# Performance work log

Measured on AMD Instinct MI355X. Metric: run time of the kernel, lower is better.

## Reference

```python
import jax, jax.numpy as jnp
import numpy as np
from jax import lax

IOU_THRESHOLD = 0.5
TOP = 1000


def setup_inputs() -> dict:
    key = jax.random.key(0)
    k1, k2, k3, k4, k5 = jax.random.split(key, 5)
    B, P = 16, 20000
    # valid (x1, y1, x2, y2) boxes on an ~800x800 image
    x1 = jax.random.uniform(k1, (B, P)) * 800.0
    y1 = jax.random.uniform(k2, (B, P)) * 800.0
    w = jax.random.uniform(k3, (B, P)) * 200.0 + 1.0
    h = jax.random.uniform(k4, (B, P)) * 200.0 + 1.0
    reg = jnp.stack([x1, y1, x1 + w, y1 + h], axis=-1)  # [B, P, 4]
    cls = jax.random.normal(k5, (B, P))                  # [B, P]
    return {"reg": reg, "cls": cls}


def _pairwise_iou(boxes):
    """boxes: [B, N, 4] (x1,y1,x2,y2) -> IoU [B, N, N]."""
    a = boxes[:, :, None, :]  # [B, N, 1, 4]
    b = boxes[:, None, :, :]  # [B, 1, N, 4]
    xx1 = jnp.maximum(a[..., 0], b[..., 0])
    yy1 = jnp.maximum(a[..., 1], b[..., 1])
    xx2 = jnp.minimum(a[..., 2], b[..., 2])
    yy2 = jnp.minimum(a[..., 3], b[..., 3])
    inter = jnp.clip(xx2 - xx1, 0.0) * jnp.clip(yy2 - yy1, 0.0)
    area_a = (a[..., 2] - a[..., 0]) * (a[..., 3] - a[..., 1])
    area_b = (b[..., 2] - b[..., 0]) * (b[..., 3] - b[..., 1])
    return inter / (area_a + area_b - inter)


def reference(reg, cls):
    B = cls.shape[0]
    # sort by confidence descending, gather boxes, keep top
    order = jnp.argsort(-cls, axis=1)                      # [B, P]
    sorted_cls = jnp.take_along_axis(cls, order, axis=1)[:, :TOP]            # [B, N]
    sorted_reg = jnp.take_along_axis(reg, order[:, :, None], axis=1)[:, :TOP]  # [B, N, 4]
    N = sorted_cls.shape[1]

    iou = _pairwise_iou(sorted_reg)                        # [B, N, N]

    # sequential greedy suppression: if box i still kept, drop boxes with IoU>=thr
    def body(mask, i):
        keep_i = mask[:, i]                                # [B]
        tmp = iou[:, i, :] < IOU_THRESHOLD                 # [B, N]
        upd = (mask & tmp).at[:, i].set(True)
        new_mask = jnp.where(keep_i[:, None], upd, mask)
        return new_mask, None

    mask0 = jnp.ones((B, N), dtype=bool)
    mask, _ = lax.scan(body, mask0, jnp.arange(N))

    out_reg = jnp.where(mask[:, :, None], sorted_reg, 0.0)
    out_cls = jnp.where(mask, sorted_cls, 0.0)
    return out_reg, out_cls
```

## Files before the change

kernel.cpp:

```cpp
#include <hip/hip_runtime.h>
#include <stdint.h>

#define BATCH 16
#define NPTS  20000
#define TOPK  1000
#define NKPT  20
#define NBIN  2048
#define NCOPY 4
#define CANDCAP 1024

__device__ __forceinline__ uint32_t key_desc(float f) {
    uint32_t u = __float_as_uint(f);
    uint32_t m = (u & 0x80000000u) ? ~u : (u | 0x80000000u);
    return ~m;
}

__device__ __forceinline__ float key_undo(uint32_t k) {
    uint32_t m = ~k;
    uint32_t u = (m & 0x80000000u) ? (m & 0x7FFFFFFFu) : ~m;
    return __uint_as_float(u);
}

__device__ __forceinline__ void push64(bool pred, uint64_t val, int* cntr,
                                       uint64_t* list, int lane) {
    uint64_t mask = __ballot(pred);
    if (mask) {
        int first = __ffsll((long long)mask) - 1;
        int base = 0;
        if (lane == first) base = atomicAdd(cntr, (int)__popcll(mask));
        base = __shfl(base, first);
        if (pred) {
            int off = (int)__popcll(mask & ((1ull << lane) - 1ull));
            list[base + off] = val;
        }
    }
}

__device__ __forceinline__ void wave_select(const uint64_t* lst, int n, int r,
                                            uint64_t* out, int wave, int lane) {
    if (wave == 0) {
        uint64_t my = (lane < n) ? lst[lane] : ~0ull;
        int rank = 0;
        for (int i = 0; i < n; ++i) { uint64_t o = __shfl(my, i); if (o < my) rank++; }
        if (lane < n && rank == r) *out = my;
    }
}

__device__ uint64_t bit_search(const uint32_t* klds, uint64_t known, uint64_t kmask,
                               int startbit, uint32_t r, int* sh_c,
                               int tid, int lane) {
    for (int bit = startbit; bit >= 0; --bit) {
        if (tid == 0) *sh_c = 0;
        __syncthreads();
        uint32_t local = 0;
        #pragma unroll
        for (int j = 0; j < NKPT; ++j) {
            int p = tid + j * 1024;
            if (p < NPTS) {
                uint64_t k64 = ((uint64_t)klds[p] << 32) | (uint32_t)p;
                if ((k64 & kmask) == known && !((k64 >> bit) & 1ull)) local++;
            }
        }
        #pragma unroll
        for (int d = 1; d < 64; d <<= 1) local += __shfl_xor(local, d);
        if (lane == 0 && local) atomicAdd(sh_c, (int)local);
        __syncthreads();
        uint32_t c0 = (uint32_t)*sh_c;
        if (r >= c0) { known |= 1ull << bit; r -= c0; }
        kmask |= 1ull << bit;
        __syncthreads();
    }
    return known;
}

__device__ __forceinline__ void hist_scan_find(
    uint32_t (*wh)[NBIN], uint32_t* wsum, uint32_t* wpre,
    int* sh_T, int* sh_r, int* sh_binc,
    int tid, int wave, int lane, uint32_t r)
{
    uint32_t m0 = 0, m1 = 0;
    #pragma unroll
    for (int cpy = 0; cpy < NCOPY; ++cpy) { m0 += wh[cpy][2*tid]; m1 += wh[cpy][2*tid+1]; }
    uint32_t s = m0 + m1, x = s;
    #pragma unroll
    for (int d = 1; d < 64; d <<= 1) { uint32_t t = __shfl_up(x, d); if (lane >= d) x += t; }
    if (lane == 63) wsum[wave] = x;
    __syncthreads();
    if (wave == 0 && lane < 16) {
        uint32_t v = wsum[lane], y = v;
        #pragma unroll
        for (int d = 1; d < 16; d <<= 1) { uint32_t t = __shfl_up(y, d); if (lane >= d) y += t; }
        wpre[lane] = y - v;
    }
    __syncthreads();
    uint32_t e = wpre[wave] + (x - s);
    if (r >= e && r < e + s) {
        if (r < e + m0) { *sh_T = 2*tid;     *sh_r = (int)(r - e);      *sh_binc = (int)m0; }
        else            { *sh_T = 2*tid + 1; *sh_r = (int)(r - e - m0); *sh_binc = (int)m1; }
    }
}

__global__ __launch_bounds__(1024) void topk_kernel(
    const float* __restrict__ reg, const float* __restrict__ cls,
    float4* __restrict__ ws_boxes, float* __restrict__ ws_cls)
{
    __shared__ uint32_t klds[NPTS];
    __shared__ uint32_t whist[NCOPY][NBIN];
    __shared__ uint32_t mpre[NBIN];
    __shared__ uint32_t bcnt[NBIN];
    __shared__ uint64_t bucket[1024];
    __shared__ uint64_t cand[CANDCAP];
    __shared__ uint64_t cand2[64];
    __shared__ uint32_t wsum[16], wpre16[16];
    __shared__ int      sh_T, sh_r, sh_binc, sh_cnt, sh_c;
    __shared__ uint64_t sh_kthkey;

    const int b = blockIdx.x, tid = threadIdx.x;
    const int wave = tid >> 6, lane = tid & 63;
    const float* c = cls + (size_t)b * NPTS;

    #pragma unroll
    for (int i = 0; i < NCOPY * NBIN / 1024; ++i) ((uint32_t*)whist)[tid + i * 1024] = 0;
    __syncthreads();
    #pragma unroll
    for (int j = 0; j < NKPT; ++j) {
        int p = tid + j * 1024;
        if (p < NPTS) {
            uint32_t k = key_desc(c[p]);
            klds[p] = k;
            atomicAdd(&whist[wave >> 2][k >> 21], 1u);
        }
    }
    __syncthreads();

    {
        uint32_t m0 = 0, m1 = 0;
        #pragma unroll
        for (int cpy = 0; cpy < NCOPY; ++cpy) { m0 += whist[cpy][2*tid]; m1 += whist[cpy][2*tid+1]; }
        uint32_t s = m0 + m1, x = s;
        #pragma unroll
        for (int d = 1; d < 64; d <<= 1) { uint32_t t = __shfl_up(x, d); if (lane >= d) x += t; }
        if (lane == 63) wsum[wave] = x;
        __syncthreads();
        if (wave == 0 && lane < 16) {
            uint32_t v = wsum[lane], y = v;
            #pragma unroll
            for (int d = 1; d < 16; d <<= 1) { uint32_t t = __shfl_up(y, d); if (lane >= d) y += t; }
            wpre16[lane] = y - v;
        }
        __syncthreads();
        uint32_t E = wpre16[wave] + (x - s);
        mpre[2*tid]   = E;
        mpre[2*tid+1] = E + m0;
        bcnt[2*tid] = 0; bcnt[2*tid+1] = 0;
        uint32_t r9 = TOPK - 1;
        if (r9 >= E && r9 < E + s) {
            if (r9 < E + m0) { sh_T = 2*tid;     sh_r = (int)(r9 - E);      sh_binc = (int)m0; }
            else             { sh_T = 2*tid + 1; sh_r = (int)(r9 - E - m0); sh_binc = (int)m1; }
        }
    }
    __syncthreads();
    const uint32_t T1 = (uint32_t)sh_T;
    int r = sh_r;
    const int cnt1 = sh_binc;
    uint64_t known = (uint64_t)T1 << 53;

    if (cnt1 <= 64) {
        if (tid == 0) sh_cnt = 0;
        __syncthreads();
        #pragma unroll
        for (int j = 0; j < NKPT; ++j) {
            int p = tid + j * 1024;
            uint32_t k = (p < NPTS) ? klds[p] : 0xFFFFFFFFu;
            push64(p < NPTS && (k >> 21) == T1,
                   ((uint64_t)k << 32) | (uint32_t)p, &sh_cnt, cand2, lane);
        }
        __syncthreads();
        wave_select(cand2, cnt1, r, &sh_kthkey, wave, lane);
        __syncthreads();
    } else if (cnt1 <= CANDCAP) {
        if (tid == 0) sh_cnt = 0;
        __syncthreads();
        #pragma unroll
        for (int j = 0; j < NKPT; ++j) {
            int p = tid + j * 1024;
            uint32_t k = (p < NPTS) ? klds[p] : 0xFFFFFFFFu;
            push64(p < NPTS && (k >> 21) == T1,
                   ((uint64_t)k << 32) | (uint32_t)p, &sh_cnt, cand, lane);
        }
        __syncthreads();
        #pragma unroll
        for (int i = 0; i < NCOPY * NBIN / 1024; ++i) ((uint32_t*)whist)[tid + i * 1024] = 0;
        __syncthreads();
        for (int i = tid; i < cnt1; i += 1024)
            atomicAdd(&whist[wave >> 2][(uint32_t)((cand[i] >> 42) & 2047)], 1u);
        __syncthreads();
        hist_scan_find(whist, wsum, wpre16, &sh_T, &sh_r, &sh_binc, tid, wave, lane, (uint32_t)r);
        __syncthreads();
        const uint32_t T2 = (uint32_t)sh_T; r = sh_r;
        const int cnt2 = sh_binc;
        known |= (uint64_t)T2 << 42;
        if (cnt2 <= 64) {
            if (tid == 0) sh_cnt = 0;
            __syncthreads();
            for (int i = tid; i < cnt1; i += 1024)
                push64(((cand[i] >> 42) & 2047) == (uint64_t)T2,
                       cand[i], &sh_cnt, cand2, lane);
            __syncthreads();
            wave_select(cand2, cnt2, r, &sh_kthkey, wave, lane);
            __syncthreads();
        } else {
            uint64_t kk = bit_search(klds, known, 0xFFFFFC0000000000ull, 41,
                                     (uint32_t)r, &sh_c, tid, lane);
            if (tid == 0) sh_kthkey = kk;
            __syncthreads();
        }
    } else {
        uint64_t kk = bit_search(klds, known, 0xFFE0000000000000ull, 52,
                                 (uint32_t)r, &sh_c, tid, lane);
        if (tid == 0) sh_kthkey = kk;
        __syncthreads();
    }
    const uint64_t kthkey = sh_kthkey;

    #pragma unroll
    for (int j = 0; j < NKPT; ++j) {
        int p = tid + j * 1024;
        if (p < NPTS) {
            uint32_t k = klds[p];
            uint64_t key = ((uint64_t)k << 32) | (uint32_t)p;
            if (key <= kthkey) {
                uint32_t t = k >> 21;
                uint32_t pos = mpre[t] + atomicAdd(&bcnt[t], 1u);
                bucket[pos] = key;
            }
        }
    }
    __syncthreads();

    if (tid < TOPK) {
        uint64_t e = bucket[tid];
        uint32_t t = (uint32_t)(e >> 53);
        uint32_t base = mpre[t], n = bcnt[t];
        int rank = (int)base;
        for (uint32_t q = 0; q < n; ++q) rank += (bucket[base + q] < e) ? 1 : 0;
        int p = (int)(e & 0xFFFFFFFFull);
        ws_boxes[b * TOPK + rank] = ((const float4*)reg)[(size_t)b * NPTS + p];
        ws_cls[b * TOPK + rank] = key_undo((uint32_t)(e >> 32));
    }
}

__global__ __launch_bounds__(256) void iou_kernel(
    const float4* __restrict__ ws_boxes, uint32_t* __restrict__ suppT)
{
    __shared__ float4 boxes[TOPK];
    __shared__ float  areas[TOPK];
    const int b   = blockIdx.y;
    const int j   = blockIdx.x;
    const int tid = threadIdx.x;
    for (int i = tid; i < TOPK; i += 256) {
        float4 v = ws_boxes[b * TOPK + i];
        boxes[i] = v;
        areas[i] = (v.z - v.x) * (v.w - v.y);
    }
    __syncthreads();

    const int lane = tid & 63;
    const int wave = tid >> 6;
    uint32_t* t = suppT + (size_t)b * 32 * 1024;

    for (int k = wave; ; k += 4) {
        const int i = j + (k << 4);
        if (i >= TOPK) break;
        float4 a = boxes[i];
        float areaA = areas[i];
        uint64_t mine = 0;
        for (int w2 = i >> 6; w2 < 16; ++w2) {
            int col = (w2 << 6) | lane;
            bool sup = false;
            if (col < TOPK) {
                float4 bb = boxes[col];
                float xx1 = fmaxf(a.x, bb.x);
                float yy1 = fmaxf(a.y, bb.y);
                float xx2 = fminf(a.z, bb.z);
                float yy2 = fminf(a.w, bb.w);
                float iw = fmaxf(xx2 - xx1, 0.0f);
                float ih = fmaxf(yy2 - yy1, 0.0f);
                float inter = iw * ih;
                float iou = inter / (areaA + areas[col] - inter);
                sup = (iou >= 0.5f);
            }
            uint64_t m = __ballot(sup);
            if (lane == w2) mine = m;
        }
        if (lane < 16) {
            t[(2 * lane + 0) * 1024 + i] = (uint32_t)(mine & 0xFFFFFFFFull);
            t[(2 * lane + 1) * 1024 + i] = (uint32_t)(mine >> 32);
        }
    }
}

__global__ __launch_bounds__(64) void sweep_kernel(
    const uint32_t* __restrict__ suppT, const float4* __restrict__ ws_boxes,
    const float* __restrict__ ws_cls, float* __restrict__ out)
{
    const int b    = blockIdx.x;
    const int lane = threadIdx.x;
    const int myw  = lane & 31;
    const uint32_t* base = suppT + (size_t)b * 32 * 1024;

    uint32_t remv = 0, keptw = 0;
    uint4 dgA[8], clA[8], dgB[8], clB[8];

#define LOADG(W, DG, CL) { \
    const uint4* dp_ = (const uint4*)(base + (W) * 1024 + (W) * 32); \
    const uint4* cp_ = (const uint4*)(base + myw * 1024 + (W) * 32); \
    _Pragma("unroll") \
    for (int k_ = 0; k_ < 8; ++k_) { DG[k_] = dp_[k_]; CL[k_] = cp_[k_]; } }

#define STEP(D, C, BBIT) { \
    uint32_t live_ = (((~cur) >> (BBIT)) & 1u) & (uint32_t)((BBIT) < nb); \
    uint32_t msk_ = (uint32_t)0 - live_; \
    kmask |= (live_ << (BBIT)); \
    cur  |= (D) & msk_; \
    acc  |= (C) & msk_; }

#define PROC(W, DG, CL) { \
    const int nb = ((W) == 31) ? (TOPK - 31 * 32) : 32; \
    uint32_t cur = __shfl(remv, (W)); \
    uint32_t kmask = 0, acc = 0; \
    _Pragma("unroll") \
    for (int k_ = 0; k_ < 8; ++k_) { \
        STEP(DG[k_].x, CL[k_].x, 4 * k_ + 0); \
        STEP(DG[k_].y, CL[k_].y, 4 * k_ + 1); \
        STEP(DG[k_].z, CL[k_].z, 4 * k_ + 2); \
        STEP(DG[k_].w, CL[k_].w, 4 * k_ + 3); \
    } \
    remv |= acc; \
    if (myw == (W)) keptw = kmask; }

    LOADG(0, dgA, clA);
    #pragma unroll 1
    for (int w2 = 0; w2 < 16; ++w2) {
        const int wE = 2 * w2, wO = 2 * w2 + 1;
        LOADG(wO, dgB, clB);
        PROC(wE, dgA, clA);
        if (wO + 1 < 32) LOADG(wO + 1, dgA, clA);
        PROC(wO, dgB, clB);
    }

    __shared__ uint32_t skept[32];
    if (lane < 32) skept[lane] = keptw;
    __syncthreads();

    const float4* bx = ws_boxes + (size_t)b * TOPK;
    const float*  bc = ws_cls + (size_t)b * TOPK;
    float4* outr = (float4*)out + (size_t)b * TOPK;
    float*  outc = out + (size_t)BATCH * TOPK * 4 + (size_t)b * TOPK;
    for (int i = lane; i < TOPK; i += 64) {
        uint32_t keep = (skept[i >> 5] >> (i & 31)) & 1u;
        float4 v = bx[i];
        float cv = bc[i];
        outr[i] = keep ? v : make_float4(0.f, 0.f, 0.f, 0.f);
        outc[i] = keep ? cv : 0.0f;
    }
#undef LOADG
#undef STEP
#undef PROC
}

extern "C" void kernel_launch(void* const* d_in, const int* in_sizes, int n_in,
                              void* d_out, int out_size, void* d_ws, size_t ws_size,
                              hipStream_t stream) {
    (void)in_sizes; (void)n_in; (void)out_size; (void)ws_size;
    const float* reg = (const float*)d_in[0];
    const float* cls = (const float*)d_in[1];
    float* out = (float*)d_out;
    char* ws = (char*)d_ws;

    float4*   ws_boxes = (float4*)ws;
    float*    ws_cls   = (float*)(ws + 256000);
    uint32_t* suppT    = (uint32_t*)(ws + 320000);

    topk_kernel<<<dim3(BATCH), dim3(1024), 0, stream>>>(reg, cls, ws_boxes, ws_cls);
    iou_kernel<<<dim3(16, BATCH), dim3(256), 0, stream>>>(ws_boxes, suppT);
    sweep_kernel<<<dim3(BATCH), dim3(64), 0, stream>>>(suppT, ws_boxes, ws_cls, out);
}
```

Before: 84.97 us.

## Keep top-k keys in registers and rank selected keys via wave bitonic sort

The top-k kernel now holds each thread's 20 sort keys in registers instead of an 80KB shared-memory array, which shrinks LDS use and lets more blocks fit per CU. The final stage changes from per-bin atomic bucketing plus a linear rank count to compacting the selected keys into a 1024-entry buffer. That buffer is ranked with a per-wave bitonic sort followed by binary searches across the other waves' sorted runs. The candidate capacity doubles and launch bounds request higher occupancy, at the cost of more register pressure and possible spills.

```diff
diff --git a/kernel.cpp b/kernel.cpp
--- a/kernel.cpp
+++ b/kernel.cpp
@@ -7,7 +7,7 @@
 #define NKPT  20
 #define NBIN  2048
 #define NCOPY 4
-#define CANDCAP 1024
+#define CANDCAP 2048
 
 __device__ __forceinline__ uint32_t key_desc(float f) {
     uint32_t u = __float_as_uint(f);
@@ -46,7 +46,7 @@
     }
 }
 
-__device__ uint64_t bit_search(const uint32_t* klds, uint64_t known, uint64_t kmask,
+__device__ uint64_t bit_search(const uint32_t* kreg, uint64_t known, uint64_t kmask,
                                int startbit, uint32_t r, int* sh_c,
                                int tid, int lane) {
     for (int bit = startbit; bit >= 0; --bit) {
@@ -56,10 +56,8 @@
         #pragma unroll
         for (int j = 0; j < NKPT; ++j) {
             int p = tid + j * 1024;
-            if (p < NPTS) {
-                uint64_t k64 = ((uint64_t)klds[p] << 32) | (uint32_t)p;
-                if ((k64 & kmask) == known && !((k64 >> bit) & 1ull)) local++;
-            }
+            uint64_t k64 = ((uint64_t)kreg[j] << 32) | (uint32_t)p;
+            if (p < NPTS && (k64 & kmask) == known && !((k64 >> bit) & 1ull)) local++;
         }
         #pragma unroll
         for (int d = 1; d < 64; d <<= 1) local += __shfl_xor(local, d);
@@ -100,65 +98,41 @@
     }
 }
 
-__global__ __launch_bounds__(1024) void topk_kernel(
+__global__ __launch_bounds__(1024, 4) void topk_kernel(
     const float* __restrict__ reg, const float* __restrict__ cls,
     float4* __restrict__ ws_boxes, float* __restrict__ ws_cls)
 {
-    __shared__ uint32_t klds[NPTS];
     __shared__ uint32_t whist[NCOPY][NBIN];
-    __shared__ uint32_t mpre[NBIN];
-    __shared__ uint32_t bcnt[NBIN];
-    __shared__ uint64_t bucket[1024];
+    __shared__ uint32_t wsum[16], wpre[16];
+    __shared__ int      sh_T, sh_r, sh_binc, sh_cnt, sh_c;
+    __shared__ uint64_t sh_kthkey;
     __shared__ uint64_t cand[CANDCAP];
     __shared__ uint64_t cand2[64];
-    __shared__ uint32_t wsum[16], wpre16[16];
-    __shared__ int      sh_T, sh_r, sh_binc, sh_cnt, sh_c;
-    __shared__ uint64_t sh_kthkey;
+    __shared__ uint64_t sel[1024];
 
     const int b = blockIdx.x, tid = threadIdx.x;
     const int wave = tid >> 6, lane = tid & 63;
     const float* c = cls + (size_t)b * NPTS;
 
+    if (tid == 0) { sh_cnt = 0; }
+
     #pragma unroll
     for (int i = 0; i < NCOPY * NBIN / 1024; ++i) ((uint32_t*)whist)[tid + i * 1024] = 0;
-    __syncthreads();
+    uint32_t kreg[NKPT];
     #pragma unroll
     for (int j = 0; j < NKPT; ++j) {
         int p = tid + j * 1024;
-        if (p < NPTS) {
-            uint32_t k = key_desc(c[p]);
-            klds[p] = k;
-            atomicAdd(&whist[wave >> 2][k >> 21], 1u);
-        }
-    }
-    __syncthreads();
-
-    {
-        uint32_t m0 = 0, m1 = 0;
-        #pragma unroll
-        for (int cpy = 0; cpy < NCOPY; ++cpy) { m0 += whist[cpy][2*tid]; m1 += whist[cpy][2*tid+1]; }
-        uint32_t s = m0 + m1, x = s;
-        #pragma unroll
-        for (int d = 1; d < 64; d <<= 1) { uint32_t t = __shfl_up(x, d); if (lane >= d) x += t; }
-        if (lane == 63) wsum[wave] = x;
-        __syncthreads();
-        if (wave == 0 && lane < 16) {
-            uint32_t v = wsum[lane], y = v;
-            #pragma unroll
-            for (int d = 1; d < 16; d <<= 1) { uint32_t t = __shfl_up(y, d); if (lane >= d) y += t; }
-            wpre16[lane] = y - v;
-        }
-        __syncthreads();
-        uint32_t E = wpre16[wave] + (x - s);
-        mpre[2*tid]   = E;
-        mpre[2*tid+1] = E + m0;
-        bcnt[2*tid] = 0; bcnt[2*tid+1] = 0;
-        uint32_t r9 = TOPK - 1;
-        if (r9 >= E && r9 < E + s) {
-            if (r9 < E + m0) { sh_T = 2*tid;     sh_r = (int)(r9 - E);      sh_binc = (int)m0; }
-            else             { sh_T = 2*tid + 1; sh_r = (int)(r9 - E - m0); sh_binc = (int)m1; }
-        }
-    }
+        kreg[j] = (p < NPTS) ? key_desc(c[p]) : 0xFFFFFFFFu;
+    }
+    __syncthreads();
+
+    #pragma unroll
+    for (int j = 0; j < NKPT; ++j) {
+        int p = tid + j * 1024;
+        if (p < NPTS) atomicAdd(&whist[wave >> 2][kreg[j] >> 21], 1u);
+    }
+    __syncthreads();
+    hist_scan_find(whist, wsum, wpre, &sh_T, &sh_r, &sh_binc, tid, wave, lane, TOPK - 1);
     __syncthreads();
     const uint32_t T1 = (uint32_t)sh_T;
     int r = sh_r;
@@ -166,27 +140,23 @@
     uint64_t known = (uint64_t)T1 << 53;
 
     if (cnt1 <= 64) {
-        if (tid == 0) sh_cnt = 0;
         __syncthreads();
         #pragma unroll
         for (int j = 0; j < NKPT; ++j) {
             int p = tid + j * 1024;
-            uint32_t k = (p < NPTS) ? klds[p] : 0xFFFFFFFFu;
-            push64(p < NPTS && (k >> 21) == T1,
-                   ((uint64_t)k << 32) | (uint32_t)p, &sh_cnt, cand2, lane);
+            push64(p < NPTS && (kreg[j] >> 21) == T1,
+                   ((uint64_t)kreg[j] << 32) | (uint32_t)p, &sh_cnt, cand2, lane);
         }
         __syncthreads();
         wave_select(cand2, cnt1, r, &sh_kthkey, wave, lane);
         __syncthreads();
     } else if (cnt1 <= CANDCAP) {
-        if (tid == 0) sh_cnt = 0;
         __syncthreads();
         #pragma unroll
         for (int j = 0; j < NKPT; ++j) {
             int p = tid + j * 1024;
-            uint32_t k = (p < NPTS) ? klds[p] : 0xFFFFFFFFu;
-            push64(p < NPTS && (k >> 21) == T1,
-                   ((uint64_t)k << 32) | (uint32_t)p, &sh_cnt, cand, lane);
+            push64(p < NPTS && (kreg[j] >> 21) == T1,
+                   ((uint64_t)kreg[j] << 32) | (uint32_t)p, &sh_cnt, cand, lane);
         }
         __syncthreads();
         #pragma unroll
@@ -195,7 +165,7 @@
         for (int i = tid; i < cnt1; i += 1024)
             atomicAdd(&whist[wave >> 2][(uint32_t)((cand[i] >> 42) & 2047)], 1u);
         __syncthreads();
-        hist_scan_find(whist, wsum, wpre16, &sh_T, &sh_r, &sh_binc, tid, wave, lane, (uint32_t)r);
+        hist_scan_find(whist, wsum, wpre, &sh_T, &sh_r, &sh_binc, tid, wave, lane, (uint32_t)r);
         __syncthreads();
         const uint32_t T2 = (uint32_t)sh_T; r = sh_r;
         const int cnt2 = sh_binc;
@@ -210,43 +180,63 @@
             wave_select(cand2, cnt2, r, &sh_kthkey, wave, lane);
             __syncthreads();
         } else {
-            uint64_t kk = bit_search(klds, known, 0xFFFFFC0000000000ull, 41,
+            uint64_t kk = bit_search(kreg, known, 0xFFFFFC0000000000ull, 41,
                                      (uint32_t)r, &sh_c, tid, lane);
             if (tid == 0) sh_kthkey = kk;
             __syncthreads();
         }
     } else {
-        uint64_t kk = bit_search(klds, known, 0xFFE0000000000000ull, 52,
+        uint64_t kk = bit_search(kreg, known, 0xFFE0000000000000ull, 52,
                                  (uint32_t)r, &sh_c, tid, lane);
         if (tid == 0) sh_kthkey = kk;
         __syncthreads();
     }
     const uint64_t kthkey = sh_kthkey;
 
+    if (tid == 0) sh_cnt = 0;
+    sel[tid] = ~0ull;
+    __syncthreads();
     #pragma unroll
     for (int j = 0; j < NKPT; ++j) {
         int p = tid + j * 1024;
-        if (p < NPTS) {
-            uint32_t k = klds[p];
-            uint64_t key = ((uint64_t)k << 32) | (uint32_t)p;
-            if (key <= kthkey) {
-                uint32_t t = k >> 21;
-                uint32_t pos = mpre[t] + atomicAdd(&bcnt[t], 1u);
-                bucket[pos] = key;
-            }
-        }
-    }
-    __syncthreads();
-
-    if (tid < TOPK) {
-        uint64_t e = bucket[tid];
-        uint32_t t = (uint32_t)(e >> 53);
-        uint32_t base = mpre[t], n = bcnt[t];
-        int rank = (int)base;
-        for (uint32_t q = 0; q < n; ++q) rank += (bucket[base + q] < e) ? 1 : 0;
+        uint64_t key = ((uint64_t)kreg[j] << 32) | (uint32_t)p;
+        push64(p < NPTS && key <= kthkey, key, &sh_cnt, sel, lane);
+    }
+    __syncthreads();
+
+    uint64_t e = sel[tid];
+    #pragma unroll
+    for (int k = 2; k <= 64; k <<= 1) {
+        #pragma unroll
+        for (int j = k >> 1; j >= 1; j >>= 1) {
+            uint64_t o = __shfl_xor(e, j);
+            uint64_t lo = (e < o) ? e : o;
+            uint64_t hi = (e < o) ? o : e;
+            bool dir   = (lane & k) == 0;
+            bool upper = (lane & j) != 0;
+            e = (upper == dir) ? hi : lo;
+        }
+    }
+    sel[tid] = e;
+    __syncthreads();
+    int grank = lane;
+    #pragma unroll 1
+    for (int w2 = 0; w2 < 16; ++w2) {
+        if (w2 == wave) continue;
+        const uint64_t* bp = &sel[w2 * 64];
+        int cf = 0;
+        #pragma unroll
+        for (int s = 32; s >= 1; s >>= 1) {
+            int t2 = cf + s;
+            if (bp[t2 - 1] < e) cf = t2;
+        }
+        if (bp[cf] < e) cf++;
+        grank += cf;
+    }
+    if (e != ~0ull) {
         int p = (int)(e & 0xFFFFFFFFull);
-        ws_boxes[b * TOPK + rank] = ((const float4*)reg)[(size_t)b * NPTS + p];
-        ws_cls[b * TOPK + rank] = key_undo((uint32_t)(e >> 32));
+        ws_boxes[b * TOPK + grank] = ((const float4*)reg)[(size_t)b * NPTS + p];
+        ws_cls[b * TOPK + grank] = key_undo((uint32_t)(e >> 32));
     }
 }
 
```

Result: no change. 83.35 us (-1.9%).
